# Optimization experiments

Measured on AMD Instinct MI355X. Metric: run time of the kernel, lower is better.

## Reference

```python
import jax, jax.numpy as jnp
import numpy as np

CHANNELS = 64
K = 3
STRIDE = 1
GROUP_CHANNELS = 2
GROUPS = CHANNELS // GROUP_CHANNELS  # 32
RED = 4
PAD = (K - 1) // 2


def setup_inputs() -> dict:
    key = jax.random.key(0)
    ks = jax.random.split(key, 6)
    x = jax.random.normal(ks[0], (8, CHANNELS, 128, 128), dtype=jnp.float32)
    w1 = jax.random.normal(ks[1], (CHANNELS // RED, CHANNELS), dtype=jnp.float32) * 0.05
    b1 = jax.random.normal(ks[2], (CHANNELS // RED,), dtype=jnp.float32) * 0.05
    prelu_a = jnp.full((1,), 0.25, dtype=jnp.float32)
    w2 = jax.random.normal(ks[3], (K * K * GROUPS, CHANNELS // RED), dtype=jnp.float32) * 0.05
    b2 = jax.random.normal(ks[4], (K * K * GROUPS,), dtype=jnp.float32) * 0.05
    return {"x": x, "w1": w1, "b1": b1, "prelu_a": prelu_a, "w2": w2, "b2": b2}


def reference(x, w1, b1, prelu_a, w2, b2):
    # stride == 1: no avgpool
    # 1x1 conv -> PReLU -> 1x1 conv to generate per-pixel kernels
    t = jnp.einsum('bchw,oc->bohw', x, w1) + b1[None, :, None, None]
    t = jnp.where(t >= 0, t, prelu_a[0] * t)  # PReLU, single shared slope
    weight = jnp.einsum('bchw,oc->bohw', t, w2) + b2[None, :, None, None]
    b, _, h, w = weight.shape
    # (b, groups, 1, k^2, h, w)
    weight = weight.reshape(b, GROUPS, 1, K * K, h, w)
    # unfold: im2col with padding 1, stride 1; channel-major (c, kh, kw) ordering like torch.nn.Unfold
    xp = jnp.pad(x, ((0, 0), (0, 0), (PAD, PAD), (PAD, PAD)))
    patches = jnp.stack(
        [xp[:, :, i:i + h, j:j + w] for i in range(K) for j in range(K)], axis=2
    )  # (b, c, k^2, h, w)
    patches = patches.reshape(b, GROUPS, GROUP_CHANNELS, K * K, h, w)
    out = (weight * patches).sum(axis=3).reshape(b, CHANNELS, h, w)
    return out
```

## Files before the change

### kernel.cpp

```cpp
#include <hip/hip_runtime.h>

#define NPIX (128 * 128)
#define CH 64
#define RMID 16
#define KK 9
#define PLANE_B 65536

typedef float v2f __attribute__((ext_vector_type(2)));

__global__ __launch_bounds__(256, 4) void invol_fused(
    const float* __restrict__ x,
    const float* __restrict__ w1,
    const float* __restrict__ b1,
    const float* __restrict__ prelu_a,
    const float* __restrict__ w2,
    const float* __restrict__ b2,
    float* __restrict__ out)
{
    const int c    = threadIdx.x & 63;
    const int rsub = threadIdx.x >> 6;

    const int L     = blockIdx.x;
    const int bq    = L & 7;
    const int go    = (L >> 3) & 3;
    const int strip = L >> 5;

    const int hq  = 4 * strip + rsub;
    const int p0  = hq * 128 + 2 * c;
    const int pb0 = 4 * p0;

    const float* xb  = x + (size_t)bq * CH * NPIX;
    const char*  xbc = (const char*)xb;

    const float rm0 = (hq > 0)   ? 1.f : 0.f;
    const float rm2 = (hq < 127) ? 1.f : 0.f;
    const float mL  = (c > 0)    ? 1.f : 0.f;
    const float mR  = (c < 63)   ? 1.f : 0.f;
    const int   ro0 = (hq > 0)   ? -512 : 0;
    const int   ro2 = (hq < 127) ?  512 : 0;

    v2f tA0[2], tA1[2], tA2[2], tE0[2], tE1[2], tE2[2];
    {
        const char* cp0 = xbc + (size_t)(2 * (8 * go)) * PLANE_B;
        const char* cp1 = cp0 + PLANE_B;
        tA0[0] = *(const v2f*)(cp0 + (size_t)(pb0 + ro0));
        tA1[0] = *(const v2f*)(cp0 + (size_t)pb0);
        tA2[0] = *(const v2f*)(cp0 + (size_t)(pb0 + ro2));
        tE0[0] = *(const v2f*)(cp1 + (size_t)(pb0 + ro0));
        tE1[0] = *(const v2f*)(cp1 + (size_t)pb0);
        tE2[0] = *(const v2f*)(cp1 + (size_t)(pb0 + ro2));
    }

    v2f t2[RMID];
#pragma unroll
    for (int r = 0; r < RMID; ++r) {
        const float b = b1[r];
        t2[r].x = b; t2[r].y = b;
    }
    const float* xp = xb + p0;
    v2f xv[2][8];
#pragma unroll
    for (int k = 0; k < 8; ++k)
        xv[0][k] = *(const v2f*)(xp + (size_t)k * NPIX);
#pragma unroll
    for (int oct = 0; oct < 8; ++oct) {
        const int cb = oct & 1, nb = cb ^ 1;
        if (oct < 7) {
#pragma unroll
            for (int k = 0; k < 8; ++k)
                xv[nb][k] = *(const v2f*)(xp + (size_t)((oct + 1) * 8 + k) * NPIX);
        }
#pragma unroll
        for (int k = 0; k < 8; ++k) {
#pragma unroll
            for (int r = 0; r < RMID; ++r) {
                const float w = w1[r * CH + oct * 8 + k];
                v2f wv; wv.x = w; wv.y = w;
                t2[r] = __builtin_elementwise_fma(wv, xv[cb][k], t2[r]);
            }
        }
    }
    {
        const float a = prelu_a[0];
        v2f av; av.x = a; av.y = a;
        v2f z;  z.x = 0.f; z.y = 0.f;
#pragma unroll
        for (int r = 0; r < RMID; ++r) {
            const v2f pos = __builtin_elementwise_max(t2[r], z);
            const v2f neg = __builtin_elementwise_min(t2[r], z);
            t2[r] = __builtin_elementwise_fma(av, neg, pos);
        }
    }

    v2f rm0v; rm0v.x = rm0; rm0v.y = rm0;
    v2f rm2v; rm2v.x = rm2; rm2v.y = rm2;

    char* obc = (char*)(out + (size_t)bq * CH * NPIX);

#pragma unroll
    for (int gi = 0; gi < 8; ++gi) {
        const int g   = 8 * go + gi;
        const int cur = gi & 1, nxt = cur ^ 1;

        const v2f A0 = tA0[cur] * rm0v;
        const v2f A1 = tA1[cur];
        const v2f A2 = tA2[cur] * rm2v;
        const v2f E0 = tE0[cur] * rm0v;
        const v2f E1 = tE1[cur];
        const v2f E2 = tE2[cur] * rm2v;

        const float lA0 = __shfl_up(A0.y, 1), rA0 = __shfl_down(A0.x, 1);
        const float lA1 = __shfl_up(A1.y, 1), rA1 = __shfl_down(A1.x, 1);
        const float lA2 = __shfl_up(A2.y, 1), rA2 = __shfl_down(A2.x, 1);
        const float lE0 = __shfl_up(E0.y, 1), rE0 = __shfl_down(E0.x, 1);
        const float lE1 = __shfl_up(E1.y, 1), rE1 = __shfl_down(E1.x, 1);
        const float lE2 = __shfl_up(E2.y, 1), rE2 = __shfl_down(E2.x, 1);

        if (gi < 7) {
            const char* np0 = xbc + (size_t)(2 * (g + 1)) * PLANE_B;
            const char* np1 = np0 + PLANE_B;
            tA0[nxt] = *(const v2f*)(np0 + (size_t)(pb0 + ro0));
            tA1[nxt] = *(const v2f*)(np0 + (size_t)pb0);
            tA2[nxt] = *(const v2f*)(np0 + (size_t)(pb0 + ro2));
            tE0[nxt] = *(const v2f*)(np1 + (size_t)(pb0 + ro0));
            tE1[nxt] = *(const v2f*)(np1 + (size_t)pb0);
            tE2[nxt] = *(const v2f*)(np1 + (size_t)(pb0 + ro2));
        }

        v2f oA; oA.x = 0.f; oA.y = 0.f;
        v2f oB = oA;
#pragma unroll
        for (int k = 0; k < KK; ++k) {
            const float* w2r = w2 + (g * KK + k) * RMID;
            const float bb = b2[g * KK + k];
            v2f acc; acc.x = bb; acc.y = bb;
#pragma unroll
            for (int r = 0; r < RMID; ++r) {
                const float w = w2r[r];
                v2f wv; wv.x = w; wv.y = w;
                acc = __builtin_elementwise_fma(wv, t2[r], acc);
            }
            if (k == 0 || k == 3 || k == 6) acc.x *= mL;
            if (k == 2 || k == 5 || k == 8) acc.y *= mR;

            const v2f Ar = (k < 3) ? A0 : (k < 6) ? A1 : A2;
            const v2f Er = (k < 3) ? E0 : (k < 6) ? E1 : E2;
            const float lA = (k < 3) ? lA0 : (k < 6) ? lA1 : lA2;
            const float rA = (k < 3) ? rA0 : (k < 6) ? rA1 : rA2;
            const float lE = (k < 3) ? lE0 : (k < 6) ? lE1 : lE2;
            const float rE = (k < 3) ? rE0 : (k < 6) ? rE1 : rE2;

            v2f tpA, tpE;
            if (k % 3 == 0)      { tpA.x = lA;   tpA.y = Ar.x;
                                   tpE.x = lE;   tpE.y = Er.x; }
            else if (k % 3 == 1) { tpA = Ar;     tpE = Er;     }
            else                 { tpA.x = Ar.y; tpA.y = rA;
                                   tpE.x = Er.y; tpE.y = rE;   }
            oA = __builtin_elementwise_fma(acc, tpA, oA);
            oB = __builtin_elementwise_fma(acc, tpE, oB);
        }

        __builtin_nontemporal_store(oA, (v2f*)(obc + (size_t)(2 * g)     * PLANE_B + pb0));
        __builtin_nontemporal_store(oB, (v2f*)(obc + (size_t)(2 * g + 1) * PLANE_B + pb0));
    }
}

extern "C" void kernel_launch(void* const* d_in, const int* in_sizes, int n_in,
                              void* d_out, int out_size, void* d_ws, size_t ws_size,
                              hipStream_t stream)
{
    const float* x  = (const float*)d_in[0];
    const float* w1 = (const float*)d_in[1];
    const float* b1 = (const float*)d_in[2];
    const float* pa = (const float*)d_in[3];
    const float* w2 = (const float*)d_in[4];
    const float* b2 = (const float*)d_in[5];
    float* out = (float*)d_out;

    hipLaunchKernelGGL(invol_fused, dim3(1024), dim3(256), 0, stream,
                       x, w1, b1, pa, w2, b2, out);
}
```

Measured before the change: 124.0 us.

## Process four pixels per thread with float4 vectors and halve the grid

Each thread now computes four adjacent pixels instead of two, using 4-wide vectors. A wave covers two image rows of 32 threads each, and the grid is halved to 512 blocks of eight rows. The intent is to spread each scalar weight load and each horizontal-neighbour shuffle over more FMAs, and to issue wider 16-byte loads and stores. Horizontal edge masking moves from the per-tap accumulator onto the shuffled neighbour values, which also handles the boundary between the two rows inside a wave. The cost is roughly doubled register use per thread (launch bounds lowered to 2) and fewer resident waves to hide memory latency.

New measurement: 128.9 us. 4.0% more time.

```diff
diff --git a/kernel.cpp b/kernel.cpp
--- a/kernel.cpp
+++ b/kernel.cpp
@@ -6,9 +6,13 @@
 #define KK 9
 #define PLANE_B 65536
 
-typedef float v2f __attribute__((ext_vector_type(2)));
+typedef float v4f __attribute__((ext_vector_type(4)));
 
-__global__ __launch_bounds__(256, 4) void invol_fused(
+static __device__ __forceinline__ v4f splat4(float s) {
+    v4f v; v.x = s; v.y = s; v.z = s; v.w = s; return v;
+}
+
+__global__ __launch_bounds__(256, 2) void invol_fused(
     const float* __restrict__ x,
     const float* __restrict__ w1,
     const float* __restrict__ b1,
@@ -17,16 +21,16 @@
     const float* __restrict__ b2,
     float* __restrict__ out)
 {
-    const int c    = threadIdx.x & 63;
-    const int rsub = threadIdx.x >> 6;
+    const int qc   = threadIdx.x & 31;
+    const int rsub = threadIdx.x >> 5;
 
     const int L     = blockIdx.x;
     const int bq    = L & 7;
     const int go    = (L >> 3) & 3;
     const int strip = L >> 5;
 
-    const int hq  = 4 * strip + rsub;
-    const int p0  = hq * 128 + 2 * c;
+    const int hq  = 8 * strip + rsub;
+    const int p0  = hq * 128 + 4 * qc;
     const int pb0 = 4 * p0;
 
     const float* xb  = x + (size_t)bq * CH * NPIX;
@@ -34,66 +38,63 @@
 
     const float rm0 = (hq > 0)   ? 1.f : 0.f;
     const float rm2 = (hq < 127) ? 1.f : 0.f;
-    const float mL  = (c > 0)    ? 1.f : 0.f;
-    const float mR  = (c < 63)   ? 1.f : 0.f;
+    const float mL  = (qc > 0)   ? 1.f : 0.f;
+    const float mR  = (qc < 31)  ? 1.f : 0.f;
     const int   ro0 = (hq > 0)   ? -512 : 0;
     const int   ro2 = (hq < 127) ?  512 : 0;
 
-    v2f tA0[2], tA1[2], tA2[2], tE0[2], tE1[2], tE2[2];
+    v4f tA0[2], tA1[2], tA2[2], tE0[2], tE1[2], tE2[2];
     {
         const char* cp0 = xbc + (size_t)(2 * (8 * go)) * PLANE_B;
         const char* cp1 = cp0 + PLANE_B;
-        tA0[0] = *(const v2f*)(cp0 + (size_t)(pb0 + ro0));
-        tA1[0] = *(const v2f*)(cp0 + (size_t)pb0);
-        tA2[0] = *(const v2f*)(cp0 + (size_t)(pb0 + ro2));
-        tE0[0] = *(const v2f*)(cp1 + (size_t)(pb0 + ro0));
-        tE1[0] = *(const v2f*)(cp1 + (size_t)pb0);
-        tE2[0] = *(const v2f*)(cp1 + (size_t)(pb0 + ro2));
+        tA0[0] = *(const v4f*)(cp0 + (size_t)(pb0 + ro0));
+        tA1[0] = *(const v4f*)(cp0 + (size_t)pb0);
+        tA2[0] = *(const v4f*)(cp0 + (size_t)(pb0 + ro2));
+        tE0[0] = *(const v4f*)(cp1 + (size_t)(pb0 + ro0));
+        tE1[0] = *(const v4f*)(cp1 + (size_t)pb0);
+        tE2[0] = *(const v4f*)(cp1 + (size_t)(pb0 + ro2));
     }
 
-    v2f t2[RMID];
+    v4f t2[RMID];
 #pragma unroll
-    for (int r = 0; r < RMID; ++r) {
-        const float b = b1[r];
-        t2[r].x = b; t2[r].y = b;
-    }
+    for (int r = 0; r < RMID; ++r)
+        t2[r] = splat4(b1[r]);
+
     const float* xp = xb + p0;
-    v2f xv[2][8];
+    v4f xv[2][8];
 #pragma unroll
     for (int k = 0; k < 8; ++k)
-        xv[0][k] = *(const v2f*)(xp + (size_t)k * NPIX);
+        xv[0][k] = *(const v4f*)(xp + (size_t)k * NPIX);
 #pragma unroll
     for (int oct = 0; oct < 8; ++oct) {
         const int cb = oct & 1, nb = cb ^ 1;
         if (oct < 7) {
 #pragma unroll
             for (int k = 0; k < 8; ++k)
-                xv[nb][k] = *(const v2f*)(xp + (size_t)((oct + 1) * 8 + k) * NPIX);
+                xv[nb][k] = *(const v4f*)(xp + (size_t)((oct + 1) * 8 + k) * NPIX);
         }
 #pragma unroll
         for (int k = 0; k < 8; ++k) {
 #pragma unroll
             for (int r = 0; r < RMID; ++r) {
                 const float w = w1[r * CH + oct * 8 + k];
-                v2f wv; wv.x = w; wv.y = w;
-                t2[r] = __builtin_elementwise_fma(wv, xv[cb][k], t2[r]);
+                t2[r] = __builtin_elementwise_fma(splat4(w), xv[cb][k], t2[r]);
             }
         }
     }
     {
-        const float a = prelu_a[0];
-        v2f av; av.x = a; av.y = a;
-        v2f z;  z.x = 0.f; z.y = 0.f;
+        const v4f av = splat4(prelu_a[0]);
+        const v4f z  = splat4(0.f);
 #pragma unroll
         for (int r = 0; r < RMID; ++r) {
-            const v2f pos = __builtin_elementwise_max(t2[r], z);
-            const v2f neg = __builtin_elementwise_min(t2[r], z);
+            const v4f pos = __builtin_elementwise_max(t2[r], z);
+            const v4f neg = __builtin_elementwise_min(t2[r], z);
             t2[r] = __builtin_elementwise_fma(av, neg, pos);
         }
     }
 
-    v2f rm0v; rm0v.x = rm0; rm0v.y = rm0;
-    v2f rm2v; rm2v.x = rm2; rm2v.y = rm2;
+    const v4f rm0v = splat4(rm0);
+    const v4f rm2v = splat4(rm2);
 
     char* obc = (char*)(out + (size_t)bq * CH * NPIX);
 
@@ -102,66 +103,66 @@
         const int g   = 8 * go + gi;
         const int cur = gi & 1, nxt = cur ^ 1;
 
-        const v2f A0 = tA0[cur] * rm0v;
-        const v2f A1 = tA1[cur];
-        const v2f A2 = tA2[cur] * rm2v;
-        const v2f E0 = tE0[cur] * rm0v;
-        const v2f E1 = tE1[cur];
-        const v2f E2 = tE2[cur] * rm2v;
+        const v4f A0 = tA0[cur] * rm0v;
+        const v4f A1 = tA1[cur];
+        const v4f A2 = tA2[cur] * rm2v;
+        const v4f E0 = tE0[cur] * rm0v;
+        const v4f E1 = tE1[cur];
+        const v4f E2 = tE2[cur] * rm2v;
 
-        const float lA0 = __shfl_up(A0.y, 1), rA0 = __shfl_down(A0.x, 1);
-        const float lA1 = __shfl_up(A1.y, 1), rA1 = __shfl_down(A1.x, 1);
-        const float lA2 = __shfl_up(A2.y, 1), rA2 = __shfl_down(A2.x, 1);
-        const float lE0 = __shfl_up(E0.y, 1), rE0 = __shfl_down(E0.x, 1);
-        const float lE1 = __shfl_up(E1.y, 1), rE1 = __shfl_down(E1.x, 1);
-        const float lE2 = __shfl_up(E2.y, 1), rE2 = __shfl_down(E2.x, 1);
+        float lA0 = __shfl_up(A0.w, 1), rA0 = __shfl_down(A0.x, 1);
+        float lA1 = __shfl_up(A1.w, 1), rA1 = __shfl_down(A1.x, 1);
+        float lA2 = __shfl_up(A2.w, 1), rA2 = __shfl_down(A2.x, 1);
+        float lE0 = __shfl_up(E0.w, 1), rE0 = __shfl_down(E0.x, 1);
+        float lE1 = __shfl_up(E1.w, 1), rE1 = __shfl_down(E1.x, 1);
+        float lE2 = __shfl_up(E2.w, 1), rE2 = __shfl_down(E2.x, 1);
+        lA0 *= mL; lA1 *= mL; lA2 *= mL; lE0 *= mL; lE1 *= mL; lE2 *= mL;
+        rA0 *= mR; rA1 *= mR; rA2 *= mR; rE0 *= mR; rE1 *= mR; rE2 *= mR;
 
         if (gi < 7) {
             const char* np0 = xbc + (size_t)(2 * (g + 1)) * PLANE_B;
             const char* np1 = np0 + PLANE_B;
-            tA0[nxt] = *(const v2f*)(np0 + (size_t)(pb0 + ro0));
-            tA1[nxt] = *(const v2f*)(np0 + (size_t)pb0);
-            tA2[nxt] = *(const v2f*)(np0 + (size_t)(pb0 + ro2));
-            tE0[nxt] = *(const v2f*)(np1 + (size_t)(pb0 + ro0));
-            tE1[nxt] = *(const v2f*)(np1 + (size_t)pb0);
-            tE2[nxt] = *(const v2f*)(np1 + (size_t)(pb0 + ro2));
+            tA0[nxt] = *(const v4f*)(np0 + (size_t)(pb0 + ro0));
+            tA1[nxt] = *(const v4f*)(np0 + (size_t)pb0);
+            tA2[nxt] = *(const v4f*)(np0 + (size_t)(pb0 + ro2));
+            tE0[nxt] = *(const v4f*)(np1 + (size_t)(pb0 + ro0));
+            tE1[nxt] = *(const v4f*)(np1 + (size_t)pb0);
+            tE2[nxt] = *(const v4f*)(np1 + (size_t)(pb0 + ro2));
         }
 
-        v2f oA; oA.x = 0.f; oA.y = 0.f;
-        v2f oB = oA;
+        v4f oA = splat4(0.f);
+        v4f oB = splat4(0.f);
 #pragma unroll
         for (int k = 0; k < KK; ++k) {
             const float* w2r = w2 + (g * KK + k) * RMID;
-            const float bb = b2[g * KK + k];
-            v2f acc; acc.x = bb; acc.y = bb;
+            v4f acc = splat4(b2[g * KK + k]);
 #pragma unroll
-            for (int r = 0; r < RMID; ++r) {
-                const float w = w2r[r];
-                v2f wv; wv.x = w; wv.y = w;
-                acc = __builtin_elementwise_fma(wv, t2[r], acc);
-            }
-            if (k == 0 || k == 3 || k == 6) acc.x *= mL;
-            if (k == 2 || k == 5 || k == 8) acc.y *= mR;
+            for (int r = 0; r < RMID; ++r)
+                acc = __builtin_elementwise_fma(splat4(w2r[r]), t2[r], acc);
 
-            const v2f Ar = (k < 3) ? A0 : (k < 6) ? A1 : A2;
-            const v2f Er = (k < 3) ? E0 : (k < 6) ? E1 : E2;
+            const v4f Ar = (k < 3) ? A0 : (k < 6) ? A1 : A2;
+            const v4f Er = (k < 3) ? E0 : (k < 6) ? E1 : E2;
             const float lA = (k < 3) ? lA0 : (k < 6) ? lA1 : lA2;
             const float rA = (k < 3) ? rA0 : (k < 6) ? rA1 : rA2;
             const float lE = (k < 3) ? lE0 : (k < 6) ? lE1 : lE2;
             const float rE = (k < 3) ? rE0 : (k < 6) ? rE1 : rE2;
 
-            v2f tpA, tpE;
-            if (k % 3 == 0)      { tpA.x = lA;   tpA.y = Ar.x;
-                                   tpE.x = lE;   tpE.y = Er.x; }
-            else if (k % 3 == 1) { tpA = Ar;     tpE = Er;     }
-            else                 { tpA.x = Ar.y; tpA.y = rA;
-                                   tpE.x = Er.y; tpE.y = rE;   }
+            v4f tpA, tpE;
+            if (k % 3 == 0) {
+                tpA.x = lA;   tpA.y = Ar.x; tpA.z = Ar.y; tpA.w = Ar.z;
+                tpE.x = lE;   tpE.y = Er.x; tpE.z = Er.y; tpE.w = Er.z;
+            } else if (k % 3 == 1) {
+                tpA = Ar;     tpE = Er;
+            } else {
+                tpA.x = Ar.y; tpA.y = Ar.z; tpA.z = Ar.w; tpA.w = rA;
+                tpE.x = Er.y; tpE.y = Er.z; tpE.z = Er.w; tpE.w = rE;
+            }
             oA = __builtin_elementwise_fma(acc, tpA, oA);
             oB = __builtin_elementwise_fma(acc, tpE, oB);
         }
 
-        __builtin_nontemporal_store(oA, (v2f*)(obc + (size_t)(2 * g)     * PLANE_B + pb0));
-        __builtin_nontemporal_store(oB, (v2f*)(obc + (size_t)(2 * g + 1) * PLANE_B + pb0));
+        __builtin_nontemporal_store(oA, (v4f*)(obc + (size_t)(2 * g)     * PLANE_B + pb0));
+        __builtin_nontemporal_store(oB, (v4f*)(obc + (size_t)(2 * g + 1) * PLANE_B + pb0));
     }
 }
 
@@ -177,6 +178,6 @@
     const float* b2 = (const float*)d_in[5];
     float* out = (float*)d_out;
 
-    hipLaunchKernelGGL(invol_fused, dim3(1024), dim3(256), 0, stream,
+    hipLaunchKernelGGL(invol_fused, dim3(512), dim3(256), 0, stream,
                        x, w1, b1, pa, w2, b2, out);
 }
```

## Hand-schedule global loads with inline asm and explicit vmcnt waits

Applied to the files above, without the earlier changes.

Replaces compiler-generated loads of x and the neighbourhood taps with inline-asm global_load_dwordx2 using a uniform base pointer and 32-bit offsets. Adds explicit s_waitcnt vmcnt waits with sched barriers so two octets of channel loads, and the next group's taps, stay in flight while the current data is consumed. The aim is to hide memory latency in what looks like a latency-bound kernel. Launch bounds are relaxed from 4 to 2 blocks per CU to allow more registers for the deeper prefetch, which may lower occupancy. Correctness now rests on the manual wait counts, since the compiler does not track the asm loads.

New measurement: 112.5 us. 9.3% less time.

```diff
diff --git a/kernel.cpp b/kernel.cpp
--- a/kernel.cpp
+++ b/kernel.cpp
@@ -8,7 +8,116 @@
 
 typedef float v2f __attribute__((ext_vector_type(2)));
 
-__global__ __launch_bounds__(256, 4) void invol_fused(
+#define ASM_LOAD2(dst, voff) \
+    asm volatile("global_load_dwordx2 %0, %1, %2" \
+                 : "=v"(dst) : "v"((uint32_t)(voff)), "s"(xbc))
+
+#define VMWAIT(N) do { \
+    asm volatile("s_waitcnt vmcnt(" #N ")" ::: "memory"); \
+    __builtin_amdgcn_sched_barrier(0); \
+} while (0)
+
+#define ISSUE8(B, oct) do { \
+    const uint32_t c0 = (uint32_t)pb0 + (uint32_t)((oct) * 8) * 65536u; \
+    ASM_LOAD2(B##0, c0); \
+    ASM_LOAD2(B##1, c0 + 1u * 65536u); \
+    ASM_LOAD2(B##2, c0 + 2u * 65536u); \
+    ASM_LOAD2(B##3, c0 + 3u * 65536u); \
+    ASM_LOAD2(B##4, c0 + 4u * 65536u); \
+    ASM_LOAD2(B##5, c0 + 5u * 65536u); \
+    ASM_LOAD2(B##6, c0 + 6u * 65536u); \
+    ASM_LOAD2(B##7, c0 + 7u * 65536u); \
+} while (0)
+
+#define FMA8(xvreg, ch) do { \
+    _Pragma("unroll") \
+    for (int r = 0; r < RMID; ++r) { \
+        const float w = w1[r * CH + (ch)]; \
+        v2f wv; wv.x = w; wv.y = w; \
+        t2[r] = __builtin_elementwise_fma(wv, (xvreg), t2[r]); \
+    } \
+} while (0)
+
+#define CONSUME8(B, oct) do { \
+    FMA8(B##0, (oct) * 8 + 0); \
+    FMA8(B##1, (oct) * 8 + 1); \
+    FMA8(B##2, (oct) * 8 + 2); \
+    FMA8(B##3, (oct) * 8 + 3); \
+    FMA8(B##4, (oct) * 8 + 4); \
+    FMA8(B##5, (oct) * 8 + 5); \
+    FMA8(B##6, (oct) * 8 + 6); \
+    FMA8(B##7, (oct) * 8 + 7); \
+} while (0)
+
+#define ISSUE_TAPS(B, gg) do { \
+    const uint32_t q0 = (uint32_t)pb0 + (uint32_t)(2 * (gg)) * 65536u; \
+    const uint32_t q1 = q0 + 65536u; \
+    ASM_LOAD2(B##A0, q0 + (uint32_t)ro0); \
+    ASM_LOAD2(B##A1, q0); \
+    ASM_LOAD2(B##A2, q0 + (uint32_t)ro2); \
+    ASM_LOAD2(B##E0, q1 + (uint32_t)ro0); \
+    ASM_LOAD2(B##E1, q1); \
+    ASM_LOAD2(B##E2, q1 + (uint32_t)ro2); \
+} while (0)
+
+__device__ __forceinline__ void group_tail(
+    int g, v2f tA0, v2f tA1, v2f tA2, v2f tE0, v2f tE1, v2f tE2,
+    float mL, float mR, v2f rm0v, v2f rm2v,
+    const v2f (&t2)[RMID], const float* __restrict__ w2,
+    const float* __restrict__ b2, char* obc, int pb0)
+{
+    const v2f A0 = tA0 * rm0v;
+    const v2f A1 = tA1;
+    const v2f A2 = tA2 * rm2v;
+    const v2f E0 = tE0 * rm0v;
+    const v2f E1 = tE1;
+    const v2f E2 = tE2 * rm2v;
+
+    const float lA0 = __shfl_up(A0.y, 1), rA0 = __shfl_down(A0.x, 1);
+    const float lA1 = __shfl_up(A1.y, 1), rA1 = __shfl_down(A1.x, 1);
+    const float lA2 = __shfl_up(A2.y, 1), rA2 = __shfl_down(A2.x, 1);
+    const float lE0 = __shfl_up(E0.y, 1), rE0 = __shfl_down(E0.x, 1);
+    const float lE1 = __shfl_up(E1.y, 1), rE1 = __shfl_down(E1.x, 1);
+    const float lE2 = __shfl_up(E2.y, 1), rE2 = __shfl_down(E2.x, 1);
+
+    v2f oA; oA.x = 0.f; oA.y = 0.f;
+    v2f oB = oA;
+#pragma unroll
+    for (int k = 0; k < KK; ++k) {
+        const float* w2r = w2 + (g * KK + k) * RMID;
+        const float bb = b2[g * KK + k];
+        v2f acc; acc.x = bb; acc.y = bb;
+#pragma unroll
+        for (int r = 0; r < RMID; ++r) {
+            const float w = w2r[r];
+            v2f wv; wv.x = w; wv.y = w;
+            acc = __builtin_elementwise_fma(wv, t2[r], acc);
+        }
+        if (k == 0 || k == 3 || k == 6) acc.x *= mL;
+        if (k == 2 || k == 5 || k == 8) acc.y *= mR;
+
+        const v2f Ar = (k < 3) ? A0 : (k < 6) ? A1 : A2;
+        const v2f Er = (k < 3) ? E0 : (k < 6) ? E1 : E2;
+        const float lA = (k < 3) ? lA0 : (k < 6) ? lA1 : lA2;
+        const float rA = (k < 3) ? rA0 : (k < 6) ? rA1 : rA2;
+        const float lE = (k < 3) ? lE0 : (k < 6) ? lE1 : lE2;
+        const float rE = (k < 3) ? rE0 : (k < 6) ? rE1 : rE2;
+
+        v2f tpA, tpE;
+        if (k % 3 == 0)      { tpA.x = lA;   tpA.y = Ar.x;
+                               tpE.x = lE;   tpE.y = Er.x; }
+        else if (k % 3 == 1) { tpA = Ar;     tpE = Er;     }
+        else                 { tpA.x = Ar.y; tpA.y = rA;
+                               tpE.x = Er.y; tpE.y = rE;   }
+        oA = __builtin_elementwise_fma(acc, tpA, oA);
+        oB = __builtin_elementwise_fma(acc, tpE, oB);
+    }
+
+    __builtin_nontemporal_store(oA, (v2f*)(obc + (size_t)(2 * g)     * PLANE_B + pb0));
+    __builtin_nontemporal_store(oB, (v2f*)(obc + (size_t)(2 * g + 1) * PLANE_B + pb0));
+}
+
+__global__ __launch_bounds__(256, 2) void invol_fused(
     const float* __restrict__ x,
     const float* __restrict__ w1,
     const float* __restrict__ b1,
@@ -39,17 +148,14 @@
     const int   ro0 = (hq > 0)   ? -512 : 0;
     const int   ro2 = (hq < 127) ?  512 : 0;
 
-    v2f tA0[2], tA1[2], tA2[2], tE0[2], tE1[2], tE2[2];
-    {
-        const char* cp0 = xbc + (size_t)(2 * (8 * go)) * PLANE_B;
-        const char* cp1 = cp0 + PLANE_B;
-        tA0[0] = *(const v2f*)(cp0 + (size_t)(pb0 + ro0));
-        tA1[0] = *(const v2f*)(cp0 + (size_t)pb0);
-        tA2[0] = *(const v2f*)(cp0 + (size_t)(pb0 + ro2));
-        tE0[0] = *(const v2f*)(cp1 + (size_t)(pb0 + ro0));
-        tE1[0] = *(const v2f*)(cp1 + (size_t)pb0);
-        tE2[0] = *(const v2f*)(cp1 + (size_t)(pb0 + ro2));
-    }
+    v2f xA0, xA1, xA2, xA3, xA4, xA5, xA6, xA7;
+    v2f xB0, xB1, xB2, xB3, xB4, xB5, xB6, xB7;
+    v2f taA0, taA1, taA2, taE0, taE1, taE2;
+    v2f tbA0, tbA1, tbA2, tbE0, tbE1, tbE2;
+
+    ISSUE_TAPS(ta, 8 * go + 0);
+    ISSUE8(xA, 0);
+    ISSUE8(xB, 1);
 
     v2f t2[RMID];
 #pragma unroll
@@ -57,29 +163,16 @@
         const float b = b1[r];
         t2[r].x = b; t2[r].y = b;
     }
-    const float* xp = xb + p0;
-    v2f xv[2][8];
-#pragma unroll
-    for (int k = 0; k < 8; ++k)
-        xv[0][k] = *(const v2f*)(xp + (size_t)k * NPIX);
-#pragma unroll
-    for (int oct = 0; oct < 8; ++oct) {
-        const int cb = oct & 1, nb = cb ^ 1;
-        if (oct < 7) {
-#pragma unroll
-            for (int k = 0; k < 8; ++k)
-                xv[nb][k] = *(const v2f*)(xp + (size_t)((oct + 1) * 8 + k) * NPIX);
-        }
-#pragma unroll
-        for (int k = 0; k < 8; ++k) {
-#pragma unroll
-            for (int r = 0; r < RMID; ++r) {
-                const float w = w1[r * CH + oct * 8 + k];
-                v2f wv; wv.x = w; wv.y = w;
-                t2[r] = __builtin_elementwise_fma(wv, xv[cb][k], t2[r]);
-            }
-        }
-    }
+
+    VMWAIT(8);  CONSUME8(xA, 0); ISSUE8(xA, 2);
+    VMWAIT(8);  CONSUME8(xB, 1); ISSUE8(xB, 3);
+    VMWAIT(8);  CONSUME8(xA, 2); ISSUE8(xA, 4);
+    VMWAIT(8);  CONSUME8(xB, 3); ISSUE8(xB, 5);
+    VMWAIT(8);  CONSUME8(xA, 4); ISSUE8(xA, 6);
+    VMWAIT(8);  CONSUME8(xB, 5); ISSUE8(xB, 7);
+    VMWAIT(8);  CONSUME8(xA, 6);
+    VMWAIT(0);  CONSUME8(xB, 7);
+
     {
         const float a = prelu_a[0];
         v2f av; av.x = a; av.y = a;
@@ -96,73 +189,24 @@
     v2f rm2v; rm2v.x = rm2; rm2v.y = rm2;
 
     char* obc = (char*)(out + (size_t)bq * CH * NPIX);
-
-#pragma unroll
-    for (int gi = 0; gi < 8; ++gi) {
-        const int g   = 8 * go + gi;
-        const int cur = gi & 1, nxt = cur ^ 1;
-
-        const v2f A0 = tA0[cur] * rm0v;
-        const v2f A1 = tA1[cur];
-        const v2f A2 = tA2[cur] * rm2v;
-        const v2f E0 = tE0[cur] * rm0v;
-        const v2f E1 = tE1[cur];
-        const v2f E2 = tE2[cur] * rm2v;
-
-        const float lA0 = __shfl_up(A0.y, 1), rA0 = __shfl_down(A0.x, 1);
-        const float lA1 = __shfl_up(A1.y, 1), rA1 = __shfl_down(A1.x, 1);
-        const float lA2 = __shfl_up(A2.y, 1), rA2 = __shfl_down(A2.x, 1);
-        const float lE0 = __shfl_up(E0.y, 1), rE0 = __shfl_down(E0.x, 1);
-        const float lE1 = __shfl_up(E1.y, 1), rE1 = __shfl_down(E1.x, 1);
-        const float lE2 = __shfl_up(E2.y, 1), rE2 = __shfl_down(E2.x, 1);
-
-        if (gi < 7) {
-            const char* np0 = xbc + (size_t)(2 * (g + 1)) * PLANE_B;
-            const char* np1 = np0 + PLANE_B;
-            tA0[nxt] = *(const v2f*)(np0 + (size_t)(pb0 + ro0));
-            tA1[nxt] = *(const v2f*)(np0 + (size_t)pb0);
-            tA2[nxt] = *(const v2f*)(np0 + (size_t)(pb0 + ro2));
-            tE0[nxt] = *(const v2f*)(np1 + (size_t)(pb0 + ro0));
-            tE1[nxt] = *(const v2f*)(np1 + (size_t)pb0);
-            tE2[nxt] = *(const v2f*)(np1 + (size_t)(pb0 + ro2));
-        }
-
-        v2f oA; oA.x = 0.f; oA.y = 0.f;
-        v2f oB = oA;
-#pragma unroll
-        for (int k = 0; k < KK; ++k) {
-            const float* w2r = w2 + (g * KK + k) * RMID;
-            const float bb = b2[g * KK + k];
-            v2f acc; acc.x = bb; acc.y = bb;
-#pragma unroll
-            for (int r = 0; r < RMID; ++r) {
-                const float w = w2r[r];
-                v2f wv; wv.x = w; wv.y = w;
-                acc = __builtin_elementwise_fma(wv, t2[r], acc);
-            }
-            if (k == 0 || k == 3 || k == 6) acc.x *= mL;
-            if (k == 2 || k == 5 || k == 8) acc.y *= mR;
-
-            const v2f Ar = (k < 3) ? A0 : (k < 6) ? A1 : A2;
-            const v2f Er = (k < 3) ? E0 : (k < 6) ? E1 : E2;
-            const float lA = (k < 3) ? lA0 : (k < 6) ? lA1 : lA2;
-            const float rA = (k < 3) ? rA0 : (k < 6) ? rA1 : rA2;
-            const float lE = (k < 3) ? lE0 : (k < 6) ? lE1 : lE2;
-            const float rE = (k < 3) ? rE0 : (k < 6) ? rE1 : rE2;
-
-            v2f tpA, tpE;
-            if (k % 3 == 0)      { tpA.x = lA;   tpA.y = Ar.x;
-                                   tpE.x = lE;   tpE.y = Er.x; }
-            else if (k % 3 == 1) { tpA = Ar;     tpE = Er;     }
-            else                 { tpA.x = Ar.y; tpA.y = rA;
-                                   tpE.x = Er.y; tpE.y = rE;   }
-            oA = __builtin_elementwise_fma(acc, tpA, oA);
-            oB = __builtin_elementwise_fma(acc, tpE, oB);
-        }
-
-        __builtin_nontemporal_store(oA, (v2f*)(obc + (size_t)(2 * g)     * PLANE_B + pb0));
-        __builtin_nontemporal_store(oB, (v2f*)(obc + (size_t)(2 * g + 1) * PLANE_B + pb0));
-    }
+    const int g0 = 8 * go;
+
+    ISSUE_TAPS(tb, g0 + 1); VMWAIT(6);
+    group_tail(g0 + 0, taA0, taA1, taA2, taE0, taE1, taE2, mL, mR, rm0v, rm2v, t2, w2, b2, obc, pb0);
+    ISSUE_TAPS(ta, g0 + 2); VMWAIT(6);
+    group_tail(g0 + 1, tbA0, tbA1, tbA2, tbE0, tbE1, tbE2, mL, mR, rm0v, rm2v, t2, w2, b2, obc, pb0);
+    ISSUE_TAPS(tb, g0 + 3); VMWAIT(6);
+    group_tail(g0 + 2, taA0, taA1, taA2, taE0, taE1, taE2, mL, mR, rm0v, rm2v, t2, w2, b2, obc, pb0);
+    ISSUE_TAPS(ta, g0 + 4); VMWAIT(6);
+    group_tail(g0 + 3, tbA0, tbA1, tbA2, tbE0, tbE1, tbE2, mL, mR, rm0v, rm2v, t2, w2, b2, obc, pb0);
+    ISSUE_TAPS(tb, g0 + 5); VMWAIT(6);
+    group_tail(g0 + 4, taA0, taA1, taA2, taE0, taE1, taE2, mL, mR, rm0v, rm2v, t2, w2, b2, obc, pb0);
+    ISSUE_TAPS(ta, g0 + 6); VMWAIT(6);
+    group_tail(g0 + 5, tbA0, tbA1, tbA2, tbE0, tbE1, tbE2, mL, mR, rm0v, rm2v, t2, w2, b2, obc, pb0);
+    ISSUE_TAPS(tb, g0 + 7); VMWAIT(6);
+    group_tail(g0 + 6, taA0, taA1, taA2, taE0, taE1, taE2, mL, mR, rm0v, rm2v, t2, w2, b2, obc, pb0);
+    VMWAIT(2);
+    group_tail(g0 + 7, tbA0, tbA1, tbA2, tbE0, tbE1, tbE2, mL, mR, rm0v, rm2v, t2, w2, b2, obc, pb0);
 }
 
 extern "C" void kernel_launch(void* const* d_in, const int* in_sizes, int n_in,
```
